# Optimization experiments

Measured on AMD Instinct MI355X. Metric: run time of the kernel, lower is better.

The kernel has to match this reference:

```python
import jax, jax.numpy as jnp
import numpy as np

D_MODEL = 256
N_LEVELS = 4
N_HEADS = 8
N_POINTS = 4
D_HEAD = D_MODEL // N_HEADS  # 32
BATCH = 8
SHAPES = np.array([[64, 64], [32, 32], [16, 16], [8, 8]], dtype=np.int32)
LEN_IN = int((SHAPES[:, 0] * SHAPES[:, 1]).sum())  # 5440
LEN_Q = LEN_IN
STARTS = np.concatenate([[0], np.cumsum(SHAPES[:, 0] * SHAPES[:, 1])[:-1]]).astype(np.int32)


def _offset_bias():
    # faithful _reset_parameters grid init for sampling_offsets bias
    thetas = np.arange(N_HEADS, dtype=np.float64) * (2.0 * np.pi / N_HEADS)
    grid = np.stack([np.cos(thetas), np.sin(thetas)], -1)
    grid = grid / np.abs(grid).max(-1, keepdims=True)
    grid = np.tile(grid[:, None, None, :], (1, N_LEVELS, N_POINTS, 1))
    grid = grid * (np.arange(N_POINTS) + 1)[None, None, :, None]
    return jnp.asarray(grid.reshape(-1), dtype=jnp.float32)


def setup_inputs() -> dict:
    key = jax.random.key(0)
    ks = jax.random.split(key, 8)
    s = 1.0 / np.sqrt(D_MODEL)
    return {
        "query": jax.random.normal(ks[0], (BATCH, LEN_Q, D_MODEL), jnp.float32),
        "reference_points": jax.random.uniform(ks[1], (BATCH, LEN_Q, N_LEVELS, 2), jnp.float32),
        "input_flatten": jax.random.normal(ks[2], (BATCH, LEN_IN, D_MODEL), jnp.float32),
        "input_spatial_shapes": jnp.asarray(SHAPES),
        "input_level_start_index": jnp.asarray(STARTS),
        "W_val": jax.random.normal(ks[3], (D_MODEL, D_MODEL), jnp.float32) * s,
        "b_val": jnp.zeros((D_MODEL,), jnp.float32),
        "W_off": jax.random.normal(ks[4], (D_MODEL, N_HEADS * N_LEVELS * N_POINTS * 2), jnp.float32) * 0.01,
        "b_off": _offset_bias(),
        "W_attn": jax.random.normal(ks[5], (D_MODEL, N_HEADS * N_LEVELS * N_POINTS), jnp.float32) * s,
        "b_attn": jnp.zeros((N_HEADS * N_LEVELS * N_POINTS,), jnp.float32),
        "W_out": jax.random.normal(ks[6], (D_MODEL, D_MODEL), jnp.float32) * s,
        "b_out": jnp.zeros((D_MODEL,), jnp.float32),
    }


def _ms_deform_attn_core(value, shapes_np, starts_np, sampling_locations, attention_weights):
    # value: (N, Lin, Hn, d); sampling_locations: (N, Lq, Hn, L, P, 2) in [0,1]
    # attention_weights: (N, Lq, Hn, L, P)
    n, lq = sampling_locations.shape[:2]
    value_t = jnp.transpose(value, (0, 2, 1, 3))  # (N, Hn, Lin, d)
    out = jnp.zeros((n, N_HEADS, lq, value.shape[-1]), value.dtype)
    for lvl in range(N_LEVELS):
        H, W = int(shapes_np[lvl, 0]), int(shapes_np[lvl, 1])
        st = int(starts_np[lvl])
        v = value_t[:, :, st:st + H * W]  # (N, Hn, H*W, d)
        loc = jnp.transpose(sampling_locations[:, :, :, lvl], (0, 2, 1, 3, 4))  # (N, Hn, Lq, P, 2)
        x = loc[..., 0] * W - 0.5
        y = loc[..., 1] * H - 0.5
        x0 = jnp.floor(x).astype(jnp.int32)
        y0 = jnp.floor(y).astype(jnp.int32)
        lx = x - x0
        ly = y - y0
        x1, y1 = x0 + 1, y0 + 1

        def gather(yc, xc):
            valid = (yc >= 0) & (yc < H) & (xc >= 0) & (xc < W)
            idx = jnp.clip(yc, 0, H - 1) * W + jnp.clip(xc, 0, W - 1)
            idx = idx.reshape(n, N_HEADS, -1)  # (N, Hn, Lq*P)
            g = jnp.take_along_axis(v, idx[..., None], axis=2)  # (N, Hn, Lq*P, d)
            return g * valid.reshape(n, N_HEADS, -1, 1)

        w00 = ((1 - lx) * (1 - ly)).reshape(n, N_HEADS, -1, 1)
        w01 = (lx * (1 - ly)).reshape(n, N_HEADS, -1, 1)
        w10 = ((1 - lx) * ly).reshape(n, N_HEADS, -1, 1)
        w11 = (lx * ly).reshape(n, N_HEADS, -1, 1)
        samp = (gather(y0, x0) * w00 + gather(y0, x1) * w01 +
                gather(y1, x0) * w10 + gather(y1, x1) * w11)
        samp = samp.reshape(n, N_HEADS, lq, N_POINTS, -1)
        aw = jnp.transpose(attention_weights[:, :, :, lvl], (0, 2, 1, 3))  # (N, Hn, Lq, P)
        out = out + (samp * aw[..., None]).sum(axis=3)
    return jnp.transpose(out, (0, 2, 1, 3)).reshape(n, lq, -1)


def reference(query, reference_points, input_flatten, input_spatial_shapes,
              input_level_start_index, W_val, b_val, W_off, b_off,
              W_attn, b_attn, W_out, b_out):
    shapes_np = np.asarray(input_spatial_shapes)
    starts_np = np.asarray(input_level_start_index)
    n, lq, _ = query.shape
    lin = input_flatten.shape[1]

    value = (input_flatten @ W_val + b_val).reshape(n, lin, N_HEADS, D_HEAD)
    off = (query @ W_off + b_off).reshape(n, lq, N_HEADS, N_LEVELS, N_POINTS, 2)
    attn = jax.nn.softmax((query @ W_attn + b_attn).reshape(n, lq, N_HEADS, N_LEVELS * N_POINTS), axis=-1)
    attn = attn.reshape(n, lq, N_HEADS, N_LEVELS, N_POINTS)

    # normalizer: (L, 2) as [W, H]
    normalizer = jnp.stack([input_spatial_shapes[:, 1], input_spatial_shapes[:, 0]], -1).astype(query.dtype)
    loc = reference_points[:, :, None, :, None, :] + off / normalizer[None, None, None, :, None, :]

    out = _ms_deform_attn_core(value, shapes_np, starts_np, loc, attn)
    return out @ W_out + b_out
```

## Files before the change

### kernel.cpp

```cpp
#include <hip/hip_runtime.h>

typedef unsigned short ushort;
typedef unsigned int uint;
typedef __bf16 bf16x8 __attribute__((ext_vector_type(8)));
typedef float floatx4 __attribute__((ext_vector_type(4)));
typedef float floatx2 __attribute__((ext_vector_type(2)));
typedef ushort ushort8 __attribute__((ext_vector_type(8)));
typedef uint uintx4 __attribute__((ext_vector_type(4)));

constexpr int LQ = 5440;
constexpr int ROWS = 43520;

__device__ __forceinline__ ushort f2b(float f) {
  union { float f; uint i; } v; v.f = f;
  uint r = v.i + 0x7FFFu + ((v.i >> 16) & 1u);
  return (ushort)(r >> 16);
}
__device__ __forceinline__ float blo(uint u) {
  union { uint i; float f; } v; v.i = u << 16; return v.f;
}
__device__ __forceinline__ float bhi(uint u) {
  union { uint i; float f; } v; v.i = u & 0xFFFF0000u; return v.f;
}
__device__ __forceinline__ void glds16(const ushort* g, ushort* l) {
  __builtin_amdgcn_global_load_lds(
      (const __attribute__((address_space(1))) void*)g,
      (__attribute__((address_space(3))) void*)l, 16, 0, 0);
}

__global__ __launch_bounds__(256) void wcast_kernel(
    const float* __restrict__ Wv, const float* __restrict__ Wo,
    const float* __restrict__ Wa, const float* __restrict__ Wu,
    ushort* __restrict__ Wt) {
  int k = threadIdx.x;
  int n = blockIdx.x;
  int m = blockIdx.y;
  const float* src = (m == 0) ? Wv : (m == 1) ? Wo : (m == 2) ? Wa : Wu;
  int N = (m == 2) ? 128 : 256;
  if (n >= N) return;
  size_t off = (size_t)m * 65536 - ((m == 3) ? 32768 : 0);
  Wt[off + (size_t)n * 256 + k] = f2b(src[(size_t)k * N + n]);
}

__device__ __forceinline__ void val_body(
    int vbx, const float* __restrict__ X, const ushort* __restrict__ WtV,
    const float* __restrict__ bval, ushort* __restrict__ value16,
    ushort* At, ushort* Bs) {
  const int t = threadIdx.x, lane = t & 63, wv = t >> 6;
  const int row_base = vbx * 64;
  floatx4 acc[4][4];
#pragma unroll
  for (int i = 0; i < 4; ++i)
#pragma unroll
    for (int j = 0; j < 4; ++j) acc[i][j] = floatx4{0.f, 0.f, 0.f, 0.f};

  const int r = t >> 2, q = t & 3;
  const float* ap = X + (size_t)(row_base + r) * 256 + q * 8;
  ushort* aslot = &At[((r >> 4) * 64 + q * 16 + (r & 15)) * 8];
  const ushort* bsrc[4];
#pragma unroll
  for (int i = 0; i < 4; ++i) {
    int l = t + 256 * i;
    int nt = l >> 6, qq = (l >> 4) & 3, n15 = l & 15;
    bsrc[i] = WtV + (size_t)(nt * 16 + n15) * 256 + qq * 8;
  }

  for (int k0 = 0; k0 < 256; k0 += 32) {
#pragma unroll
    for (int i = 0; i < 4; ++i) glds16(bsrc[i] + k0, &Bs[(t + 256 * i) * 8]);
    {
      float4 a0 = *(const float4*)(ap + k0), a1 = *(const float4*)(ap + k0 + 4);
      ushort8 u;
      u[0] = f2b(a0.x); u[1] = f2b(a0.y); u[2] = f2b(a0.z); u[3] = f2b(a0.w);
      u[4] = f2b(a1.x); u[5] = f2b(a1.y); u[6] = f2b(a1.z); u[7] = f2b(a1.w);
      *(ushort8*)aslot = u;
    }
    __syncthreads();
    bf16x8 af[4], bf[4];
#pragma unroll
    for (int ti = 0; ti < 4; ++ti)
      af[ti] = *(const bf16x8*)&At[(ti * 64 + lane) * 8];
#pragma unroll
    for (int tj = 0; tj < 4; ++tj)
      bf[tj] = *(const bf16x8*)&Bs[((4 * wv + tj) * 64 + lane) * 8];
#pragma unroll
    for (int ti = 0; ti < 4; ++ti)
#pragma unroll
      for (int tj = 0; tj < 4; ++tj)
        acc[ti][tj] = __builtin_amdgcn_mfma_f32_16x16x32_bf16(af[ti], bf[tj], acc[ti][tj], 0, 0, 0);
    __syncthreads();
  }
  const int quad = lane >> 4, l15 = lane & 15;
#pragma unroll
  for (int tj = 0; tj < 4; ++tj) {
    int gcol = (4 * wv + tj) * 16 + l15;
    float b = bval[gcol];
#pragma unroll
    for (int ti = 0; ti < 4; ++ti)
#pragma unroll
      for (int reg = 0; reg < 4; ++reg) {
        int grow = row_base + ti * 16 + quad * 4 + reg;
        value16[(size_t)grow * 256 + gcol] = f2b(acc[ti][tj][reg] + b);
      }
  }
}

__device__ __forceinline__ void oa_body(
    int obx, const float* __restrict__ Q, const ushort* __restrict__ WtOA,
    const float* __restrict__ boff, const float* __restrict__ battn,
    const float* __restrict__ refp, uint4* __restrict__ tblq,
    ushort* At, ushort* Bs) {
  const int t = threadIdx.x;
  const int lane = t & 63, wv = t >> 6;
  const int quad = lane >> 4, l15 = lane & 15;
  const int row_base = (obx % 680) * 64;
  const int hp = obx / 680;
  floatx4 accO[4], accA[2];
#pragma unroll
  for (int p = 0; p < 4; ++p) accO[p] = floatx4{0.f, 0.f, 0.f, 0.f};
#pragma unroll
  for (int q = 0; q < 2; ++q) accA[q] = floatx4{0.f, 0.f, 0.f, 0.f};

  const int r = t >> 2, q = t & 3;
  const float* ap = Q + (size_t)(row_base + r) * 256 + q * 8;
  ushort* aslot = &At[((r >> 4) * 64 + q * 16 + (r & 15)) * 8];
  const ushort* osrc0;
  const ushort* osrc1 = nullptr;
  {
    int nt = t >> 6, qq = (t >> 4) & 3, n15 = t & 15;
    int nr = nt * 16 + n15;
    int grow_ = (nr < 64) ? (hp * 64 + nr) : (256 + hp * 32 + (nr - 64));
    osrc0 = WtOA + (size_t)grow_ * 256 + qq * 8;
  }
  if (t < 128) {
    int l = t + 256;
    int nt = l >> 6, qq = (l >> 4) & 3, n15 = l & 15;
    int nr = nt * 16 + n15;
    int grow_ = 256 + hp * 32 + (nr - 64);
    osrc1 = WtOA + (size_t)grow_ * 256 + qq * 8;
  }

  for (int k0 = 0; k0 < 256; k0 += 32) {
    glds16(osrc0 + k0, &Bs[t * 8]);
    if (t < 128) glds16(osrc1 + k0, &Bs[(t + 256) * 8]);
    {
      float4 a0 = *(const float4*)(ap + k0), a1 = *(const float4*)(ap + k0 + 4);
      ushort8 u;
      u[0] = f2b(a0.x); u[1] = f2b(a0.y); u[2] = f2b(a0.z); u[3] = f2b(a0.w);
      u[4] = f2b(a1.x); u[5] = f2b(a1.y); u[6] = f2b(a1.z); u[7] = f2b(a1.w);
      *(ushort8*)aslot = u;
    }
    __syncthreads();
    bf16x8 af = *(const bf16x8*)&At[(wv * 64 + lane) * 8];
#pragma unroll
    for (int p = 0; p < 4; ++p) {
      bf16x8 bf = *(const bf16x8*)&Bs[(p * 64 + lane) * 8];
      accO[p] = __builtin_amdgcn_mfma_f32_16x16x32_bf16(af, bf, accO[p], 0, 0, 0);
    }
#pragma unroll
    for (int qk = 0; qk < 2; ++qk) {
      bf16x8 bf = *(const bf16x8*)&Bs[((4 + qk) * 64 + lane) * 8];
      accA[qk] = __builtin_amdgcn_mfma_f32_16x16x32_bf16(af, bf, accA[qk], 0, 0, 0);
    }
    __syncthreads();
  }

  const int lp = l15, l = lp >> 2;
  const int wd = 64 >> l;
  const int st = (l == 0) ? 0 : (l == 1) ? 4096 : (l == 2) ? 5120 : 5376;
  const float lw = (float)wd;
  const int src = (quad << 4) | (2 * (lp & 7));
  float boO[4], boA[2];
#pragma unroll
  for (int p = 0; p < 4; ++p) boO[p] = boff[(4 * hp + p) * 16 + l15];
#pragma unroll
  for (int qk = 0; qk < 2; ++qk) boA[qk] = battn[(2 * hp + qk) * 16 + l15];

#pragma unroll
  for (int reg = 0; reg < 4; ++reg) {
    int grow = row_base + wv * 16 + quad * 4 + reg;
    float rx = refp[(size_t)grow * 8 + l * 2];
    float ry = refp[(size_t)grow * 8 + l * 2 + 1];
#pragma unroll
    for (int hh = 0; hh < 2; ++hh) {
      int h = 2 * hp + hh;
      float xa = accA[hh][reg] + boA[hh];
      float m = xa;
      m = fmaxf(m, __shfl_xor(m, 1, 64));
      m = fmaxf(m, __shfl_xor(m, 2, 64));
      m = fmaxf(m, __shfl_xor(m, 4, 64));
      m = fmaxf(m, __shfl_xor(m, 8, 64));
      float e = __expf(xa - m);
      float ssum = e;
      ssum += __shfl_xor(ssum, 1, 64);
      ssum += __shfl_xor(ssum, 2, 64);
      ssum += __shfl_xor(ssum, 4, 64);
      ssum += __shfl_xor(ssum, 8, 64);
      float aw = e / ssum;
      float v0 = accO[2 * hh][reg] + boO[2 * hh];
      float v1 = accO[2 * hh + 1][reg] + boO[2 * hh + 1];
      float x_lo = __shfl(v0, src, 64),     x_hi = __shfl(v1, src, 64);
      float y_lo = __shfl(v0, src | 1, 64), y_hi = __shfl(v1, src | 1, 64);
      float xo = (lp < 8) ? x_lo : x_hi;
      float yo = (lp < 8) ? y_lo : y_hi;
      float X = rx * lw + xo - 0.5f;
      float Y = ry * lw + yo - 0.5f;
      float fx = floorf(X), fy = floorf(Y);
      float lx = X - fx, ly = Y - fy;
      int x0 = (int)fx, y0 = (int)fy, x1 = x0 + 1, y1 = y0 + 1;
      int cx0 = min(max(x0, 0), wd - 1), cx1 = min(max(x1, 0), wd - 1);
      int cy0 = min(max(y0, 0), wd - 1), cy1 = min(max(y1, 0), wd - 1);
      float vx0 = (x0 >= 0 && x0 < wd) ? 1.f : 0.f;
      float vx1 = (x1 >= 0 && x1 < wd) ? 1.f : 0.f;
      float vy0 = (y0 >= 0 && y0 < wd) ? 1.f : 0.f;
      float vy1 = (y1 >= 0 && y1 < wd) ? 1.f : 0.f;
      float g00 = (1.f - lx) * (1.f - ly) * vx0 * vy0 * aw;
      float g01 = lx * (1.f - ly) * vx1 * vy0 * aw;
      float g10 = (1.f - lx) * ly * vx0 * vy1 * aw;
      float g11 = lx * ly * vx1 * vy1 * aw;
      uint i00 = st + cy0 * wd + cx0, i01 = st + cy0 * wd + cx1;
      uint i10 = st + cy1 * wd + cx0, i11 = st + cy1 * wd + cx1;
      uint4 ov;
      ov.x = i00 | (i01 << 16);
      ov.y = i10 | (i11 << 16);
      ov.z = (uint)f2b(g00) | ((uint)f2b(g01) << 16);
      ov.w = (uint)f2b(g10) | ((uint)f2b(g11) << 16);
      tblq[((size_t)grow * 8 + h) * 16 + lp] = ov;
    }
  }
}

__global__ __launch_bounds__(256) void valoa_kernel(
    const float* __restrict__ X, const float* __restrict__ Q,
    const ushort* __restrict__ Wt,
    const float* __restrict__ bval, const float* __restrict__ boff,
    const float* __restrict__ battn, const float* __restrict__ refp,
    ushort* __restrict__ value16, uint4* __restrict__ tblq) {
  __shared__ ushort At[2048];
  __shared__ ushort Bs[8192];
  const int bx = blockIdx.x;
  const int q5 = bx / 5, r5 = bx % 5;
  if (r5 == 0)
    val_body(q5, X, Wt, bval, value16, At, Bs);
  else
    oa_body(q5 * 4 + r5 - 1, Q, Wt + 65536, boff, battn, refp, tblq, At, Bs);
}

__global__ __launch_bounds__(512) void core_kernel(
    const ushort* __restrict__ value16, const uint4* __restrict__ tblq,
    uint* __restrict__ coreo32) {
  const int bx = blockIdx.x;
  const int b = bx & 7;
  const int pr = bx >> 3;
  const int brow0 = b * LQ + pr * 2;
  const int t = threadIdx.x;
  const int h = t >> 6, lane = t & 63;
  const int s = lane >> 3, g = lane & 7;
  const size_t sb = ((size_t)brow0 * 8 + h) * 16;
  uint4 sA0 = tblq[sb + s];
  uint4 sA1 = tblq[sb + 8 + s];
  uint4 sB0 = tblq[sb + 128 + s];
  uint4 sB1 = tblq[sb + 136 + s];
  const uint2* vb = (const uint2*)value16 + (size_t)b * (LQ * 64) + h * 8 + g;
  float a[4] = {0.f, 0.f, 0.f, 0.f};
  float c[4] = {0.f, 0.f, 0.f, 0.f};

  auto proc = [&](const uint4& sl, float* ac) {
    uint2 v00 = vb[(size_t)(sl.x & 0xFFFFu) * 64];
    uint2 v01 = vb[(size_t)(sl.x >> 16) * 64];
    uint2 v10 = vb[(size_t)(sl.y & 0xFFFFu) * 64];
    uint2 v11 = vb[(size_t)(sl.y >> 16) * 64];
    float w00 = blo(sl.z), w01 = bhi(sl.z), w10 = blo(sl.w), w11 = bhi(sl.w);
    ac[0] = fmaf(w00, blo(v00.x), ac[0]); ac[1] = fmaf(w00, bhi(v00.x), ac[1]);
    ac[2] = fmaf(w00, blo(v00.y), ac[2]); ac[3] = fmaf(w00, bhi(v00.y), ac[3]);
    ac[0] = fmaf(w01, blo(v01.x), ac[0]); ac[1] = fmaf(w01, bhi(v01.x), ac[1]);
    ac[2] = fmaf(w01, blo(v01.y), ac[2]); ac[3] = fmaf(w01, bhi(v01.y), ac[3]);
    ac[0] = fmaf(w10, blo(v10.x), ac[0]); ac[1] = fmaf(w10, bhi(v10.x), ac[1]);
    ac[2] = fmaf(w10, blo(v10.y), ac[2]); ac[3] = fmaf(w10, bhi(v10.y), ac[3]);
    ac[0] = fmaf(w11, blo(v11.x), ac[0]); ac[1] = fmaf(w11, bhi(v11.x), ac[1]);
    ac[2] = fmaf(w11, blo(v11.y), ac[2]); ac[3] = fmaf(w11, bhi(v11.y), ac[3]);
  };
  proc(sA0, a); proc(sA1, a);
  proc(sB0, c); proc(sB1, c);

#pragma unroll
  for (int m = 8; m <= 32; m <<= 1) {
#pragma unroll
    for (int i = 0; i < 4; ++i) {
      a[i] += __shfl_xor(a[i], m, 64);
      c[i] += __shfl_xor(c[i], m, 64);
    }
  }
  if (s == 0) {
    uint2 o0, o1;
    o0.x = (uint)f2b(a[0]) | ((uint)f2b(a[1]) << 16);
    o0.y = (uint)f2b(a[2]) | ((uint)f2b(a[3]) << 16);
    o1.x = (uint)f2b(c[0]) | ((uint)f2b(c[1]) << 16);
    o1.y = (uint)f2b(c[2]) | ((uint)f2b(c[3]) << 16);
    *(uint2*)(coreo32 + (size_t)brow0 * 128 + h * 16 + g * 2) = o0;
    *(uint2*)(coreo32 + (size_t)(brow0 + 1) * 128 + h * 16 + g * 2) = o1;
  }
}

__global__ __launch_bounds__(256) void gemm_out64(
    const ushort* __restrict__ C, const ushort* __restrict__ WtU,
    const float* __restrict__ bout, float* __restrict__ out) {
  __shared__ ushort At[2048];
  __shared__ ushort Bs[8192];
  const int t = threadIdx.x, lane = t & 63, wv = t >> 6;
  const int row_base = blockIdx.x * 64;
  floatx4 acc[4][4];
#pragma unroll
  for (int i = 0; i < 4; ++i)
#pragma unroll
    for (int j = 0; j < 4; ++j) acc[i][j] = floatx4{0.f, 0.f, 0.f, 0.f};

  const ushort* asrc;
  {
    int mt = t >> 6, qq = (t >> 4) & 3, r15 = t & 15;
    asrc = C + (size_t)(row_base + mt * 16 + r15) * 256 + qq * 8;
  }
  const ushort* bsrc[4];
#pragma unroll
  for (int i = 0; i < 4; ++i) {
    int l = t + 256 * i;
    int nt = l >> 6, qq = (l >> 4) & 3, n15 = l & 15;
    bsrc[i] = WtU + (size_t)(nt * 16 + n15) * 256 + qq * 8;
  }

  for (int k0 = 0; k0 < 256; k0 += 32) {
    glds16(asrc + k0, &At[t * 8]);
#pragma unroll
    for (int i = 0; i < 4; ++i) glds16(bsrc[i] + k0, &Bs[(t + 256 * i) * 8]);
    __syncthreads();
    bf16x8 af[4], bf[4];
#pragma unroll
    for (int ti = 0; ti < 4; ++ti)
      af[ti] = *(const bf16x8*)&At[(ti * 64 + lane) * 8];
#pragma unroll
    for (int tj = 0; tj < 4; ++tj)
      bf[tj] = *(const bf16x8*)&Bs[((4 * wv + tj) * 64 + lane) * 8];
#pragma unroll
    for (int ti = 0; ti < 4; ++ti)
#pragma unroll
      for (int tj = 0; tj < 4; ++tj)
        acc[ti][tj] = __builtin_amdgcn_mfma_f32_16x16x32_bf16(af[ti], bf[tj], acc[ti][tj], 0, 0, 0);
    __syncthreads();
  }
  const int quad = lane >> 4, l15 = lane & 15;
#pragma unroll
  for (int tj = 0; tj < 4; ++tj) {
    int gcol = (4 * wv + tj) * 16 + l15;
    float b = bout[gcol];
#pragma unroll
    for (int ti = 0; ti < 4; ++ti)
#pragma unroll
      for (int reg = 0; reg < 4; ++reg) {
        int grow = row_base + ti * 16 + quad * 4 + reg;
        out[(size_t)grow * 256 + gcol] = acc[ti][tj][reg] + b;
      }
  }
}

extern "C" void kernel_launch(void* const* d_in, const int* in_sizes, int n_in,
                              void* d_out, int out_size, void* d_ws, size_t ws_size,
                              hipStream_t stream) {
  const float* query  = (const float*)d_in[0];
  const float* refp   = (const float*)d_in[1];
  const float* inpf   = (const float*)d_in[2];
  const float* W_val  = (const float*)d_in[5];
  const float* b_val  = (const float*)d_in[6];
  const float* W_off  = (const float*)d_in[7];
  const float* b_off  = (const float*)d_in[8];
  const float* W_attn = (const float*)d_in[9];
  const float* b_attn = (const float*)d_in[10];
  const float* W_out  = (const float*)d_in[11];
  const float* b_out  = (const float*)d_in[12];

  char* ws = (char*)d_ws;
  ushort* Wt    = (ushort*)ws;
  ushort* value = (ushort*)(ws + 1048576);
  uint4*  tbl   = (uint4*)(ws + 23330816);
  ushort* coreo = (ushort*)(ws + 112459776);

  dim3 blk(256);
  wcast_kernel<<<dim3(256, 4), blk, 0, stream>>>(W_val, W_off, W_attn, W_out, Wt);
  valoa_kernel<<<dim3(3400), blk, 0, stream>>>(inpf, query, Wt, b_val, b_off,
                                               b_attn, refp, value, tbl);
  core_kernel <<<dim3(21760), dim3(512), 0, stream>>>(value, tbl, (uint*)coreo);
  gemm_out64  <<<dim3(680), blk, 0, stream>>>(coreo, Wt + 163840, b_out, (float*)d_out);
}
```

Measured before the change: 346.0 us.

## Store value per-head contiguous and gather horizontal pixel pairs with 16-byte loads

```diff
diff --git a/kernel.cpp b/kernel.cpp
--- a/kernel.cpp
+++ b/kernel.cpp
@@ -4,9 +4,7 @@
 typedef unsigned int uint;
 typedef __bf16 bf16x8 __attribute__((ext_vector_type(8)));
 typedef float floatx4 __attribute__((ext_vector_type(4)));
-typedef float floatx2 __attribute__((ext_vector_type(2)));
 typedef ushort ushort8 __attribute__((ext_vector_type(8)));
-typedef uint uintx4 __attribute__((ext_vector_type(4)));
 
 constexpr int LQ = 5440;
 constexpr int ROWS = 43520;
@@ -42,12 +40,16 @@
   Wt[off + (size_t)n * 256 + k] = f2b(src[(size_t)k * N + n]);
 }
 
-__device__ __forceinline__ void val_body(
-    int vbx, const float* __restrict__ X, const ushort* __restrict__ WtV,
-    const float* __restrict__ bval, ushort* __restrict__ value16,
-    ushort* At, ushort* Bs) {
+__global__ __launch_bounds__(256) void gemm_val64(
+    const float* __restrict__ X, const ushort* __restrict__ WtV,
+    const float* __restrict__ bval, ushort* __restrict__ value16) {
+  __shared__ ushort At[2048];
+  __shared__ ushort Bs[8192];
   const int t = threadIdx.x, lane = t & 63, wv = t >> 6;
+  const int vbx = blockIdx.x;
   const int row_base = vbx * 64;
+  const int bb = vbx / 85;
+  const int idx_base = (vbx - bb * 85) * 64;
   floatx4 acc[4][4];
 #pragma unroll
   for (int i = 0; i < 4; ++i)
@@ -94,27 +96,31 @@
 #pragma unroll
   for (int tj = 0; tj < 4; ++tj) {
     int gcol = (4 * wv + tj) * 16 + l15;
+    int hh = gcol >> 5, cc = gcol & 31;
     float b = bval[gcol];
 #pragma unroll
     for (int ti = 0; ti < 4; ++ti)
 #pragma unroll
       for (int reg = 0; reg < 4; ++reg) {
-        int grow = row_base + ti * 16 + quad * 4 + reg;
-        value16[(size_t)grow * 256 + gcol] = f2b(acc[ti][tj][reg] + b);
+        int idx = idx_base + ti * 16 + quad * 4 + reg;
+        value16[(((size_t)bb * 8 + hh) * 5440 + idx) * 32 + cc] =
+            f2b(acc[ti][tj][reg] + b);
       }
   }
 }
 
-__device__ __forceinline__ void oa_body(
-    int obx, const float* __restrict__ Q, const ushort* __restrict__ WtOA,
+__global__ __launch_bounds__(256) void gemm_oa_kernel(
+    const float* __restrict__ Q, const ushort* __restrict__ WtOA,
     const float* __restrict__ boff, const float* __restrict__ battn,
-    const float* __restrict__ refp, uint4* __restrict__ tblq,
-    ushort* At, ushort* Bs) {
+    const float* __restrict__ refp, uint4* __restrict__ tblq) {
+  __shared__ ushort At[2048];
+  __shared__ ushort Bs[3072];
   const int t = threadIdx.x;
   const int lane = t & 63, wv = t >> 6;
   const int quad = lane >> 4, l15 = lane & 15;
-  const int row_base = (obx % 680) * 64;
-  const int hp = obx / 680;
+  const int bx = blockIdx.x;
+  const int row_base = (bx % 680) * 64;
+  const int hp = bx / 680;
   floatx4 accO[4], accA[2];
 #pragma unroll
   for (int p = 0; p < 4; ++p) accO[p] = floatx4{0.f, 0.f, 0.f, 0.f};
@@ -218,32 +224,19 @@
       float g01 = lx * (1.f - ly) * vx1 * vy0 * aw;
       float g10 = (1.f - lx) * ly * vx0 * vy1 * aw;
       float g11 = lx * ly * vx1 * vy1 * aw;
-      uint i00 = st + cy0 * wd + cx0, i01 = st + cy0 * wd + cx1;
-      uint i10 = st + cy1 * wd + cx0, i11 = st + cy1 * wd + cx1;
+      int i00 = st + cy0 * wd + cx0, i01 = st + cy0 * wd + cx1;
+      int i10 = st + cy1 * wd + cx0, i11 = st + cy1 * wd + cx1;
+      bool xv = (x0 >= 0) && (x0 < wd);
+      int pb0 = xv ? i00 : (i01 - 1);
+      int pb1 = xv ? i10 : (i11 - 1);
       uint4 ov;
-      ov.x = i00 | (i01 << 16);
-      ov.y = i10 | (i11 << 16);
+      ov.x = (uint)(pb0 + 1) | ((uint)(pb1 + 1) << 16);
+      ov.y = 0u;
       ov.z = (uint)f2b(g00) | ((uint)f2b(g01) << 16);
       ov.w = (uint)f2b(g10) | ((uint)f2b(g11) << 16);
       tblq[((size_t)grow * 8 + h) * 16 + lp] = ov;
     }
   }
-}
-
-__global__ __launch_bounds__(256) void valoa_kernel(
-    const float* __restrict__ X, const float* __restrict__ Q,
-    const ushort* __restrict__ Wt,
-    const float* __restrict__ bval, const float* __restrict__ boff,
-    const float* __restrict__ battn, const float* __restrict__ refp,
-    ushort* __restrict__ value16, uint4* __restrict__ tblq) {
-  __shared__ ushort At[2048];
-  __shared__ ushort Bs[8192];
-  const int bx = blockIdx.x;
-  const int q5 = bx / 5, r5 = bx % 5;
-  if (r5 == 0)
-    val_body(q5, X, Wt, bval, value16, At, Bs);
-  else
-    oa_body(q5 * 4 + r5 - 1, Q, Wt + 65536, boff, battn, refp, tblq, At, Bs);
 }
 
 __global__ __launch_bounds__(512) void core_kernel(
@@ -261,44 +254,50 @@
   uint4 sA1 = tblq[sb + 8 + s];
   uint4 sB0 = tblq[sb + 128 + s];
   uint4 sB1 = tblq[sb + 136 + s];
-  const uint2* vb = (const uint2*)value16 + (size_t)b * (LQ * 64) + h * 8 + g;
-  float a[4] = {0.f, 0.f, 0.f, 0.f};
-  float c[4] = {0.f, 0.f, 0.f, 0.f};
+  const char* vbm = (const char*)value16 +
+                    (((size_t)(b * 8 + h) * 5440 - 1) << 6) + (g << 4);
+  float a[8], c[8];
+#pragma unroll
+  for (int i = 0; i < 8; ++i) { a[i] = 0.f; c[i] = 0.f; }
 
   auto proc = [&](const uint4& sl, float* ac) {
-    uint2 v00 = vb[(size_t)(sl.x & 0xFFFFu) * 64];
-    uint2 v01 = vb[(size_t)(sl.x >> 16) * 64];
-    uint2 v10 = vb[(size_t)(sl.y & 0xFFFFu) * 64];
-    uint2 v11 = vb[(size_t)(sl.y >> 16) * 64];
-    float w00 = blo(sl.z), w01 = bhi(sl.z), w10 = blo(sl.w), w11 = bhi(sl.w);
-    ac[0] = fmaf(w00, blo(v00.x), ac[0]); ac[1] = fmaf(w00, bhi(v00.x), ac[1]);
-    ac[2] = fmaf(w00, blo(v00.y), ac[2]); ac[3] = fmaf(w00, bhi(v00.y), ac[3]);
-    ac[0] = fmaf(w01, blo(v01.x), ac[0]); ac[1] = fmaf(w01, bhi(v01.x), ac[1]);
-    ac[2] = fmaf(w01, blo(v01.y), ac[2]); ac[3] = fmaf(w01, bhi(v01.y), ac[3]);
-    ac[0] = fmaf(w10, blo(v10.x), ac[0]); ac[1] = fmaf(w10, bhi(v10.x), ac[1]);
-    ac[2] = fmaf(w10, blo(v10.y), ac[2]); ac[3] = fmaf(w10, bhi(v10.y), ac[3]);
-    ac[0] = fmaf(w11, blo(v11.x), ac[0]); ac[1] = fmaf(w11, bhi(v11.x), ac[1]);
-    ac[2] = fmaf(w11, blo(v11.y), ac[2]); ac[3] = fmaf(w11, bhi(v11.y), ac[3]);
+    uint b0 = sl.x & 0xFFFFu, b1 = sl.x >> 16;
+    uint4 p0 = *(const uint4*)(vbm + ((size_t)b0 << 6));
+    uint4 p1 = *(const uint4*)(vbm + ((size_t)b1 << 6));
+    float w0 = (g < 4) ? blo(sl.z) : bhi(sl.z);
+    float w1 = (g < 4) ? blo(sl.w) : bhi(sl.w);
+    ac[0] = fmaf(w0, blo(p0.x), ac[0]); ac[1] = fmaf(w0, bhi(p0.x), ac[1]);
+    ac[2] = fmaf(w0, blo(p0.y), ac[2]); ac[3] = fmaf(w0, bhi(p0.y), ac[3]);
+    ac[4] = fmaf(w0, blo(p0.z), ac[4]); ac[5] = fmaf(w0, bhi(p0.z), ac[5]);
+    ac[6] = fmaf(w0, blo(p0.w), ac[6]); ac[7] = fmaf(w0, bhi(p0.w), ac[7]);
+    ac[0] = fmaf(w1, blo(p1.x), ac[0]); ac[1] = fmaf(w1, bhi(p1.x), ac[1]);
+    ac[2] = fmaf(w1, blo(p1.y), ac[2]); ac[3] = fmaf(w1, bhi(p1.y), ac[3]);
+    ac[4] = fmaf(w1, blo(p1.z), ac[4]); ac[5] = fmaf(w1, bhi(p1.z), ac[5]);
+    ac[6] = fmaf(w1, blo(p1.w), ac[6]); ac[7] = fmaf(w1, bhi(p1.w), ac[7]);
   };
   proc(sA0, a); proc(sA1, a);
   proc(sB0, c); proc(sB1, c);
 
 #pragma unroll
-  for (int m = 8; m <= 32; m <<= 1) {
-#pragma unroll
-    for (int i = 0; i < 4; ++i) {
+  for (int m = 4; m <= 32; m <<= 1) {
+#pragma unroll
+    for (int i = 0; i < 8; ++i) {
       a[i] += __shfl_xor(a[i], m, 64);
       c[i] += __shfl_xor(c[i], m, 64);
     }
   }
-  if (s == 0) {
-    uint2 o0, o1;
+  if (s == 0 && g < 4) {
+    uint4 o0, o1;
     o0.x = (uint)f2b(a[0]) | ((uint)f2b(a[1]) << 16);
     o0.y = (uint)f2b(a[2]) | ((uint)f2b(a[3]) << 16);
+    o0.z = (uint)f2b(a[4]) | ((uint)f2b(a[5]) << 16);
+    o0.w = (uint)f2b(a[6]) | ((uint)f2b(a[7]) << 16);
     o1.x = (uint)f2b(c[0]) | ((uint)f2b(c[1]) << 16);
     o1.y = (uint)f2b(c[2]) | ((uint)f2b(c[3]) << 16);
-    *(uint2*)(coreo32 + (size_t)brow0 * 128 + h * 16 + g * 2) = o0;
-    *(uint2*)(coreo32 + (size_t)(brow0 + 1) * 128 + h * 16 + g * 2) = o1;
+    o1.z = (uint)f2b(c[4]) | ((uint)f2b(c[5]) << 16);
+    o1.w = (uint)f2b(c[6]) | ((uint)f2b(c[7]) << 16);
+    *(uint4*)(coreo32 + (size_t)brow0 * 128 + h * 16 + g * 4) = o0;
+    *(uint4*)(coreo32 + (size_t)(brow0 + 1) * 128 + h * 16 + g * 4) = o1;
   }
 }
 
@@ -385,8 +384,8 @@
 
   dim3 blk(256);
   wcast_kernel<<<dim3(256, 4), blk, 0, stream>>>(W_val, W_off, W_attn, W_out, Wt);
-  valoa_kernel<<<dim3(3400), blk, 0, stream>>>(inpf, query, Wt, b_val, b_off,
-                                               b_attn, refp, value, tbl);
+  gemm_val64  <<<dim3(680), blk, 0, stream>>>(inpf, Wt, b_val, value);
+  gemm_oa_kernel<<<dim3(2720), blk, 0, stream>>>(query, Wt + 65536, b_off, b_attn, refp, tbl);
   core_kernel <<<dim3(21760), dim3(512), 0, stream>>>(value, tbl, (uint*)coreo);
   gemm_out64  <<<dim3(680), blk, 0, stream>>>(coreo, Wt + 163840, b_out, (float*)d_out);
 }
```

Result: slower. 354.0 us (+2.3%).

## Split fused value/offset GEMM, pre-cast query to bf16, halve GEMM row tiles

Applied to the files above, without the earlier changes.

```diff
diff --git a/kernel.cpp b/kernel.cpp
--- a/kernel.cpp
+++ b/kernel.cpp
@@ -4,9 +4,7 @@
 typedef unsigned int uint;
 typedef __bf16 bf16x8 __attribute__((ext_vector_type(8)));
 typedef float floatx4 __attribute__((ext_vector_type(4)));
-typedef float floatx2 __attribute__((ext_vector_type(2)));
 typedef ushort ushort8 __attribute__((ext_vector_type(8)));
-typedef uint uintx4 __attribute__((ext_vector_type(4)));
 
 constexpr int LQ = 5440;
 constexpr int ROWS = 43520;
@@ -42,21 +40,37 @@
   Wt[off + (size_t)n * 256 + k] = f2b(src[(size_t)k * N + n]);
 }
 
-__device__ __forceinline__ void val_body(
-    int vbx, const float* __restrict__ X, const ushort* __restrict__ WtV,
-    const float* __restrict__ bval, ushort* __restrict__ value16,
-    ushort* At, ushort* Bs) {
+__global__ __launch_bounds__(256) void qcast_kernel(
+    const float* __restrict__ Q, ushort* __restrict__ Qb) {
+  int u = blockIdx.x * 256 + threadIdx.x;
+  const float4* s = (const float4*)Q + (size_t)u * 2;
+  float4 a0 = s[0], a1 = s[1];
+  ushort8 o;
+  o[0] = f2b(a0.x); o[1] = f2b(a0.y); o[2] = f2b(a0.z); o[3] = f2b(a0.w);
+  o[4] = f2b(a1.x); o[5] = f2b(a1.y); o[6] = f2b(a1.z); o[7] = f2b(a1.w);
+  *(ushort8*)(Qb + (size_t)u * 8) = o;
+}
+
+__global__ __launch_bounds__(256) void gemm_val64(
+    const float* __restrict__ X, const ushort* __restrict__ WtV,
+    const float* __restrict__ bval, ushort* __restrict__ value16) {
+  __shared__ ushort At[1024];
+  __shared__ ushort Bs[8192];
   const int t = threadIdx.x, lane = t & 63, wv = t >> 6;
-  const int row_base = vbx * 64;
-  floatx4 acc[4][4];
-#pragma unroll
-  for (int i = 0; i < 4; ++i)
+  const int row_base = blockIdx.x * 32;
+  floatx4 acc[2][4];
+#pragma unroll
+  for (int i = 0; i < 2; ++i)
 #pragma unroll
     for (int j = 0; j < 4; ++j) acc[i][j] = floatx4{0.f, 0.f, 0.f, 0.f};
 
-  const int r = t >> 2, q = t & 3;
-  const float* ap = X + (size_t)(row_base + r) * 256 + q * 8;
-  ushort* aslot = &At[((r >> 4) * 64 + q * 16 + (r & 15)) * 8];
+  const float* ap = nullptr;
+  ushort* aslot = nullptr;
+  if (t < 128) {
+    int r = t >> 2, q = t & 3;
+    ap = X + (size_t)(row_base + r) * 256 + q * 8;
+    aslot = &At[((r >> 4) * 64 + q * 16 + (r & 15)) * 8];
+  }
   const ushort* bsrc[4];
 #pragma unroll
   for (int i = 0; i < 4; ++i) {
@@ -68,7 +82,7 @@
   for (int k0 = 0; k0 < 256; k0 += 32) {
 #pragma unroll
     for (int i = 0; i < 4; ++i) glds16(bsrc[i] + k0, &Bs[(t + 256 * i) * 8]);
-    {
+    if (t < 128) {
       float4 a0 = *(const float4*)(ap + k0), a1 = *(const float4*)(ap + k0 + 4);
       ushort8 u;
       u[0] = f2b(a0.x); u[1] = f2b(a0.y); u[2] = f2b(a0.z); u[3] = f2b(a0.w);
@@ -76,15 +90,15 @@
       *(ushort8*)aslot = u;
     }
     __syncthreads();
-    bf16x8 af[4], bf[4];
-#pragma unroll
-    for (int ti = 0; ti < 4; ++ti)
+    bf16x8 af[2], bf[4];
+#pragma unroll
+    for (int ti = 0; ti < 2; ++ti)
       af[ti] = *(const bf16x8*)&At[(ti * 64 + lane) * 8];
 #pragma unroll
     for (int tj = 0; tj < 4; ++tj)
       bf[tj] = *(const bf16x8*)&Bs[((4 * wv + tj) * 64 + lane) * 8];
 #pragma unroll
-    for (int ti = 0; ti < 4; ++ti)
+    for (int ti = 0; ti < 2; ++ti)
 #pragma unroll
       for (int tj = 0; tj < 4; ++tj)
         acc[ti][tj] = __builtin_amdgcn_mfma_f32_16x16x32_bf16(af[ti], bf[tj], acc[ti][tj], 0, 0, 0);
@@ -96,7 +110,7 @@
     int gcol = (4 * wv + tj) * 16 + l15;
     float b = bval[gcol];
 #pragma unroll
-    for (int ti = 0; ti < 4; ++ti)
+    for (int ti = 0; ti < 2; ++ti)
 #pragma unroll
       for (int reg = 0; reg < 4; ++reg) {
         int grow = row_base + ti * 16 + quad * 4 + reg;
@@ -105,25 +119,29 @@
   }
 }
 
-__device__ __forceinline__ void oa_body(
-    int obx, const float* __restrict__ Q, const ushort* __restrict__ WtOA,
+__global__ __launch_bounds__(256) void gemm_oa_kernel(
+    const ushort* __restrict__ Qb, const ushort* __restrict__ WtOA,
     const float* __restrict__ boff, const float* __restrict__ battn,
-    const float* __restrict__ refp, uint4* __restrict__ tblq,
-    ushort* At, ushort* Bs) {
+    const float* __restrict__ refp, uint4* __restrict__ tblq) {
+  __shared__ ushort At[2048];
+  __shared__ ushort Bs[3072];
   const int t = threadIdx.x;
   const int lane = t & 63, wv = t >> 6;
   const int quad = lane >> 4, l15 = lane & 15;
-  const int row_base = (obx % 680) * 64;
-  const int hp = obx / 680;
+  const int bx = blockIdx.x;
+  const int row_base = (bx % 680) * 64;
+  const int hp = bx / 680;
   floatx4 accO[4], accA[2];
 #pragma unroll
   for (int p = 0; p < 4; ++p) accO[p] = floatx4{0.f, 0.f, 0.f, 0.f};
 #pragma unroll
   for (int q = 0; q < 2; ++q) accA[q] = floatx4{0.f, 0.f, 0.f, 0.f};
 
-  const int r = t >> 2, q = t & 3;
-  const float* ap = Q + (size_t)(row_base + r) * 256 + q * 8;
-  ushort* aslot = &At[((r >> 4) * 64 + q * 16 + (r & 15)) * 8];
+  const ushort* asrc;
+  {
+    int rt = t >> 6, qq = (t >> 4) & 3, r15 = t & 15;
+    asrc = Qb + (size_t)(row_base + rt * 16 + r15) * 256 + qq * 8;
+  }
   const ushort* osrc0;
   const ushort* osrc1 = nullptr;
   {
@@ -141,15 +159,9 @@
   }
 
   for (int k0 = 0; k0 < 256; k0 += 32) {
+    glds16(asrc + k0, &At[t * 8]);
     glds16(osrc0 + k0, &Bs[t * 8]);
     if (t < 128) glds16(osrc1 + k0, &Bs[(t + 256) * 8]);
-    {
-      float4 a0 = *(const float4*)(ap + k0), a1 = *(const float4*)(ap + k0 + 4);
-      ushort8 u;
-      u[0] = f2b(a0.x); u[1] = f2b(a0.y); u[2] = f2b(a0.z); u[3] = f2b(a0.w);
-      u[4] = f2b(a1.x); u[5] = f2b(a1.y); u[6] = f2b(a1.z); u[7] = f2b(a1.w);
-      *(ushort8*)aslot = u;
-    }
     __syncthreads();
     bf16x8 af = *(const bf16x8*)&At[(wv * 64 + lane) * 8];
 #pragma unroll
@@ -185,12 +197,7 @@
     for (int hh = 0; hh < 2; ++hh) {
       int h = 2 * hp + hh;
       float xa = accA[hh][reg] + boA[hh];
-      float m = xa;
-      m = fmaxf(m, __shfl_xor(m, 1, 64));
-      m = fmaxf(m, __shfl_xor(m, 2, 64));
-      m = fmaxf(m, __shfl_xor(m, 4, 64));
-      m = fmaxf(m, __shfl_xor(m, 8, 64));
-      float e = __expf(xa - m);
+      float e = __expf(xa);
       float ssum = e;
       ssum += __shfl_xor(ssum, 1, 64);
       ssum += __shfl_xor(ssum, 2, 64);
@@ -230,22 +237,6 @@
   }
 }
 
-__global__ __launch_bounds__(256) void valoa_kernel(
-    const float* __restrict__ X, const float* __restrict__ Q,
-    const ushort* __restrict__ Wt,
-    const float* __restrict__ bval, const float* __restrict__ boff,
-    const float* __restrict__ battn, const float* __restrict__ refp,
-    ushort* __restrict__ value16, uint4* __restrict__ tblq) {
-  __shared__ ushort At[2048];
-  __shared__ ushort Bs[8192];
-  const int bx = blockIdx.x;
-  const int q5 = bx / 5, r5 = bx % 5;
-  if (r5 == 0)
-    val_body(q5, X, Wt, bval, value16, At, Bs);
-  else
-    oa_body(q5 * 4 + r5 - 1, Q, Wt + 65536, boff, battn, refp, tblq, At, Bs);
-}
-
 __global__ __launch_bounds__(512) void core_kernel(
     const ushort* __restrict__ value16, const uint4* __restrict__ tblq,
     uint* __restrict__ coreo32) {
@@ -305,20 +296,20 @@
 __global__ __launch_bounds__(256) void gemm_out64(
     const ushort* __restrict__ C, const ushort* __restrict__ WtU,
     const float* __restrict__ bout, float* __restrict__ out) {
-  __shared__ ushort At[2048];
+  __shared__ ushort At[1024];
   __shared__ ushort Bs[8192];
   const int t = threadIdx.x, lane = t & 63, wv = t >> 6;
-  const int row_base = blockIdx.x * 64;
-  floatx4 acc[4][4];
-#pragma unroll
-  for (int i = 0; i < 4; ++i)
+  const int row_base = blockIdx.x * 32;
+  floatx4 acc[2][4];
+#pragma unroll
+  for (int i = 0; i < 2; ++i)
 #pragma unroll
     for (int j = 0; j < 4; ++j) acc[i][j] = floatx4{0.f, 0.f, 0.f, 0.f};
 
-  const ushort* asrc;
-  {
-    int mt = t >> 6, qq = (t >> 4) & 3, r15 = t & 15;
-    asrc = C + (size_t)(row_base + mt * 16 + r15) * 256 + qq * 8;
+  const ushort* asrc = nullptr;
+  if (t < 128) {
+    int rt = t >> 6, qq = (t >> 4) & 3, r15 = t & 15;
+    asrc = C + (size_t)(row_base + rt * 16 + r15) * 256 + qq * 8;
   }
   const ushort* bsrc[4];
 #pragma unroll
@@ -329,19 +320,19 @@
   }
 
   for (int k0 = 0; k0 < 256; k0 += 32) {
-    glds16(asrc + k0, &At[t * 8]);
+    if (t < 128) glds16(asrc + k0, &At[t * 8]);
 #pragma unroll
     for (int i = 0; i < 4; ++i) glds16(bsrc[i] + k0, &Bs[(t + 256 * i) * 8]);
     __syncthreads();
-    bf16x8 af[4], bf[4];
-#pragma unroll
-    for (int ti = 0; ti < 4; ++ti)
+    bf16x8 af[2], bf[4];
+#pragma unroll
+    for (int ti = 0; ti < 2; ++ti)
       af[ti] = *(const bf16x8*)&At[(ti * 64 + lane) * 8];
 #pragma unroll
     for (int tj = 0; tj < 4; ++tj)
       bf[tj] = *(const bf16x8*)&Bs[((4 * wv + tj) * 64 + lane) * 8];
 #pragma unroll
-    for (int ti = 0; ti < 4; ++ti)
+    for (int ti = 0; ti < 2; ++ti)
 #pragma unroll
       for (int tj = 0; tj < 4; ++tj)
         acc[ti][tj] = __builtin_amdgcn_mfma_f32_16x16x32_bf16(af[ti], bf[tj], acc[ti][tj], 0, 0, 0);
@@ -353,7 +344,7 @@
     int gcol = (4 * wv + tj) * 16 + l15;
     float b = bout[gcol];
 #pragma unroll
-    for (int ti = 0; ti < 4; ++ti)
+    for (int ti = 0; ti < 2; ++ti)
 #pragma unroll
       for (int reg = 0; reg < 4; ++reg) {
         int grow = row_base + ti * 16 + quad * 4 + reg;
@@ -379,14 +370,16 @@
 
   char* ws = (char*)d_ws;
   ushort* Wt    = (ushort*)ws;
-  ushort* value = (ushort*)(ws + 1048576);
-  uint4*  tbl   = (uint4*)(ws + 23330816);
-  ushort* coreo = (ushort*)(ws + 112459776);
+  ushort* Qb    = (ushort*)(ws + 1048576);
+  ushort* value = (ushort*)(ws + 23330816);
+  uint4*  tbl   = (uint4*)(ws + 45613056);
+  ushort* coreo = Qb;
 
   dim3 blk(256);
   wcast_kernel<<<dim3(256, 4), blk, 0, stream>>>(W_val, W_off, W_attn, W_out, Wt);
-  valoa_kernel<<<dim3(3400), blk, 0, stream>>>(inpf, query, Wt, b_val, b_off,
-                                               b_attn, refp, value, tbl);
+  qcast_kernel<<<dim3(5440), blk, 0, stream>>>(query, Qb);
+  gemm_val64  <<<dim3(1360), blk, 0, stream>>>(inpf, Wt, b_val, value);
+  gemm_oa_kernel<<<dim3(2720), blk, 0, stream>>>(Qb, Wt + 65536, b_off, b_attn, refp, tbl);
   core_kernel <<<dim3(21760), dim3(512), 0, stream>>>(value, tbl, (uint*)coreo);
-  gemm_out64  <<<dim3(680), blk, 0, stream>>>(coreo, Wt + 163840, b_out, (float*)d_out);
-}
+  gemm_out64  <<<dim3(1360), blk, 0, stream>>>(coreo, Wt + 163840, b_out, (float*)d_out);
+}
```

Measured after the change: 357.0 us. +3.2%, slower.

## Split fused value/offset GEMM kernel and compute all heads per offset block

Applied to the files above, without the earlier changes.

```diff
diff --git a/kernel.cpp b/kernel.cpp
--- a/kernel.cpp
+++ b/kernel.cpp
@@ -4,9 +4,7 @@
 typedef unsigned int uint;
 typedef __bf16 bf16x8 __attribute__((ext_vector_type(8)));
 typedef float floatx4 __attribute__((ext_vector_type(4)));
-typedef float floatx2 __attribute__((ext_vector_type(2)));
 typedef ushort ushort8 __attribute__((ext_vector_type(8)));
-typedef uint uintx4 __attribute__((ext_vector_type(4)));
 
 constexpr int LQ = 5440;
 constexpr int ROWS = 43520;
@@ -42,12 +40,13 @@
   Wt[off + (size_t)n * 256 + k] = f2b(src[(size_t)k * N + n]);
 }
 
-__device__ __forceinline__ void val_body(
-    int vbx, const float* __restrict__ X, const ushort* __restrict__ WtV,
-    const float* __restrict__ bval, ushort* __restrict__ value16,
-    ushort* At, ushort* Bs) {
+__global__ __launch_bounds__(256) void gemm_val64(
+    const float* __restrict__ X, const ushort* __restrict__ WtV,
+    const float* __restrict__ bval, ushort* __restrict__ value16) {
+  __shared__ ushort At[2048];
+  __shared__ ushort Bs[8192];
   const int t = threadIdx.x, lane = t & 63, wv = t >> 6;
-  const int row_base = vbx * 64;
+  const int row_base = blockIdx.x * 64;
   floatx4 acc[4][4];
 #pragma unroll
   for (int i = 0; i < 4; ++i)
@@ -105,44 +104,36 @@
   }
 }
 
-__device__ __forceinline__ void oa_body(
-    int obx, const float* __restrict__ Q, const ushort* __restrict__ WtOA,
+__global__ __launch_bounds__(256) void gemm_oa_kernel(
+    const float* __restrict__ Q, const ushort* __restrict__ WtOA,
     const float* __restrict__ boff, const float* __restrict__ battn,
-    const float* __restrict__ refp, uint4* __restrict__ tblq,
-    ushort* At, ushort* Bs) {
+    const float* __restrict__ refp, uint4* __restrict__ tblq) {
+  __shared__ ushort At[2048];
+  __shared__ ushort Bs[12288];
   const int t = threadIdx.x;
   const int lane = t & 63, wv = t >> 6;
   const int quad = lane >> 4, l15 = lane & 15;
-  const int row_base = (obx % 680) * 64;
-  const int hp = obx / 680;
-  floatx4 accO[4], accA[2];
-#pragma unroll
-  for (int p = 0; p < 4; ++p) accO[p] = floatx4{0.f, 0.f, 0.f, 0.f};
-#pragma unroll
-  for (int q = 0; q < 2; ++q) accA[q] = floatx4{0.f, 0.f, 0.f, 0.f};
+  const int row_base = blockIdx.x * 64;
+  floatx4 accO[16], accA[8];
+#pragma unroll
+  for (int p = 0; p < 16; ++p) accO[p] = floatx4{0.f, 0.f, 0.f, 0.f};
+#pragma unroll
+  for (int qk = 0; qk < 8; ++qk) accA[qk] = floatx4{0.f, 0.f, 0.f, 0.f};
 
   const int r = t >> 2, q = t & 3;
   const float* ap = Q + (size_t)(row_base + r) * 256 + q * 8;
   ushort* aslot = &At[((r >> 4) * 64 + q * 16 + (r & 15)) * 8];
-  const ushort* osrc0;
-  const ushort* osrc1 = nullptr;
-  {
-    int nt = t >> 6, qq = (t >> 4) & 3, n15 = t & 15;
-    int nr = nt * 16 + n15;
-    int grow_ = (nr < 64) ? (hp * 64 + nr) : (256 + hp * 32 + (nr - 64));
-    osrc0 = WtOA + (size_t)grow_ * 256 + qq * 8;
-  }
-  if (t < 128) {
-    int l = t + 256;
+  const ushort* bsrc[6];
+#pragma unroll
+  for (int i = 0; i < 6; ++i) {
+    int l = t + 256 * i;
     int nt = l >> 6, qq = (l >> 4) & 3, n15 = l & 15;
-    int nr = nt * 16 + n15;
-    int grow_ = 256 + hp * 32 + (nr - 64);
-    osrc1 = WtOA + (size_t)grow_ * 256 + qq * 8;
+    bsrc[i] = WtOA + (size_t)(nt * 16 + n15) * 256 + qq * 8;
   }
 
   for (int k0 = 0; k0 < 256; k0 += 32) {
-    glds16(osrc0 + k0, &Bs[t * 8]);
-    if (t < 128) glds16(osrc1 + k0, &Bs[(t + 256) * 8]);
+#pragma unroll
+    for (int i = 0; i < 6; ++i) glds16(bsrc[i] + k0, &Bs[(t + 256 * i) * 8]);
     {
       float4 a0 = *(const float4*)(ap + k0), a1 = *(const float4*)(ap + k0 + 4);
       ushort8 u;
@@ -153,13 +144,13 @@
     __syncthreads();
     bf16x8 af = *(const bf16x8*)&At[(wv * 64 + lane) * 8];
 #pragma unroll
-    for (int p = 0; p < 4; ++p) {
+    for (int p = 0; p < 16; ++p) {
       bf16x8 bf = *(const bf16x8*)&Bs[(p * 64 + lane) * 8];
       accO[p] = __builtin_amdgcn_mfma_f32_16x16x32_bf16(af, bf, accO[p], 0, 0, 0);
     }
 #pragma unroll
-    for (int qk = 0; qk < 2; ++qk) {
-      bf16x8 bf = *(const bf16x8*)&Bs[((4 + qk) * 64 + lane) * 8];
+    for (int qk = 0; qk < 8; ++qk) {
+      bf16x8 bf = *(const bf16x8*)&Bs[((16 + qk) * 64 + lane) * 8];
       accA[qk] = __builtin_amdgcn_mfma_f32_16x16x32_bf16(af, bf, accA[qk], 0, 0, 0);
     }
     __syncthreads();
@@ -170,11 +161,11 @@
   const int st = (l == 0) ? 0 : (l == 1) ? 4096 : (l == 2) ? 5120 : 5376;
   const float lw = (float)wd;
   const int src = (quad << 4) | (2 * (lp & 7));
-  float boO[4], boA[2];
-#pragma unroll
-  for (int p = 0; p < 4; ++p) boO[p] = boff[(4 * hp + p) * 16 + l15];
-#pragma unroll
-  for (int qk = 0; qk < 2; ++qk) boA[qk] = battn[(2 * hp + qk) * 16 + l15];
+  float boO[16], boA[8];
+#pragma unroll
+  for (int p = 0; p < 16; ++p) boO[p] = boff[p * 16 + l15];
+#pragma unroll
+  for (int qk = 0; qk < 8; ++qk) boA[qk] = battn[qk * 16 + l15];
 
 #pragma unroll
   for (int reg = 0; reg < 4; ++reg) {
@@ -182,9 +173,8 @@
     float rx = refp[(size_t)grow * 8 + l * 2];
     float ry = refp[(size_t)grow * 8 + l * 2 + 1];
 #pragma unroll
-    for (int hh = 0; hh < 2; ++hh) {
-      int h = 2 * hp + hh;
-      float xa = accA[hh][reg] + boA[hh];
+    for (int h = 0; h < 8; ++h) {
+      float xa = accA[h][reg] + boA[h];
       float m = xa;
       m = fmaxf(m, __shfl_xor(m, 1, 64));
       m = fmaxf(m, __shfl_xor(m, 2, 64));
@@ -197,8 +187,8 @@
       ssum += __shfl_xor(ssum, 4, 64);
       ssum += __shfl_xor(ssum, 8, 64);
       float aw = e / ssum;
-      float v0 = accO[2 * hh][reg] + boO[2 * hh];
-      float v1 = accO[2 * hh + 1][reg] + boO[2 * hh + 1];
+      float v0 = accO[2 * h][reg] + boO[2 * h];
+      float v1 = accO[2 * h + 1][reg] + boO[2 * h + 1];
       float x_lo = __shfl(v0, src, 64),     x_hi = __shfl(v1, src, 64);
       float y_lo = __shfl(v0, src | 1, 64), y_hi = __shfl(v1, src | 1, 64);
       float xo = (lp < 8) ? x_lo : x_hi;
@@ -230,22 +220,6 @@
   }
 }
 
-__global__ __launch_bounds__(256) void valoa_kernel(
-    const float* __restrict__ X, const float* __restrict__ Q,
-    const ushort* __restrict__ Wt,
-    const float* __restrict__ bval, const float* __restrict__ boff,
-    const float* __restrict__ battn, const float* __restrict__ refp,
-    ushort* __restrict__ value16, uint4* __restrict__ tblq) {
-  __shared__ ushort At[2048];
-  __shared__ ushort Bs[8192];
-  const int bx = blockIdx.x;
-  const int q5 = bx / 5, r5 = bx % 5;
-  if (r5 == 0)
-    val_body(q5, X, Wt, bval, value16, At, Bs);
-  else
-    oa_body(q5 * 4 + r5 - 1, Q, Wt + 65536, boff, battn, refp, tblq, At, Bs);
-}
-
 __global__ __launch_bounds__(512) void core_kernel(
     const ushort* __restrict__ value16, const uint4* __restrict__ tblq,
     uint* __restrict__ coreo32) {
@@ -385,8 +359,8 @@
 
   dim3 blk(256);
   wcast_kernel<<<dim3(256, 4), blk, 0, stream>>>(W_val, W_off, W_attn, W_out, Wt);
-  valoa_kernel<<<dim3(3400), blk, 0, stream>>>(inpf, query, Wt, b_val, b_off,
-                                               b_attn, refp, value, tbl);
+  gemm_val64  <<<dim3(680), blk, 0, stream>>>(inpf, Wt, b_val, value);
+  gemm_oa_kernel<<<dim3(680), blk, 0, stream>>>(query, Wt + 65536, b_off, b_attn, refp, tbl);
   core_kernel <<<dim3(21760), dim3(512), 0, stream>>>(value, tbl, (uint*)coreo);
   gemm_out64  <<<dim3(680), blk, 0, stream>>>(coreo, Wt + 163840, b_out, (float*)d_out);
 }
```

After: 349.8 us. About the same (+1.1%).
